# Optimization experiments

Hardware: AMD Instinct MI355X
Metric: run time of the kernel (lower is better)

Reference implementation:

```python
import jax, jax.numpy as jnp
import numpy as np

S = 4096      # total packed sequence length (8 images x 512 patches)
D = 1152      # hidden_dim
H = 16        # num_heads
HD = D // H   # head_dim = 72
MLPD = 4304   # mlp_dim
EPS = 1e-5


def setup_inputs() -> dict:
    key = jax.random.key(0)
    ks = jax.random.split(key, 16)
    f32 = jnp.float32
    w = lambda k, shp: (jax.random.normal(k, shp, f32) * 0.02)
    hidden_states = jax.random.normal(ks[0], (S, D), f32)
    cu_seqlens = (jnp.arange(9, dtype=jnp.int32) * (S // 8))  # [0,512,...,4096]
    angles = jax.random.uniform(ks[1], (S, HD // 2), f32, 0.0, 2.0 * np.pi)
    rope_cos = jnp.cos(angles)
    rope_sin = jnp.sin(angles)
    return {
        "hidden_states": hidden_states,
        "cu_seqlens": cu_seqlens,
        "rope_cos": rope_cos,
        "rope_sin": rope_sin,
        "norm0_scale": jnp.ones((D,), f32),
        "norm0_bias": jnp.zeros((D,), f32),
        "wqkv_w": w(ks[2], (D, 3 * D)),
        "wqkv_b": jnp.zeros((3 * D,), f32),
        "wo_w": w(ks[3], (D, D)),
        "wo_b": jnp.zeros((D,), f32),
        "norm1_scale": jnp.ones((D,), f32),
        "norm1_bias": jnp.zeros((D,), f32),
        "fc0_w": w(ks[4], (D, MLPD)),
        "fc0_b": jnp.zeros((MLPD,), f32),
        "fc1_w": w(ks[5], (MLPD, D)),
        "fc1_b": jnp.zeros((D,), f32),
    }


def _layernorm(x, scale, bias):
    m = jnp.mean(x, axis=-1, keepdims=True)
    v = jnp.mean(jnp.square(x - m), axis=-1, keepdims=True)
    return (x - m) * jax.lax.rsqrt(v + EPS) * scale + bias


def _rope(x, cos, sin):
    # x: (S, H, HD). Complex multiply (x0 + i x1) * (cos + i sin) in real form.
    xr = x.reshape(S, H, HD // 2, 2)
    x0, x1 = xr[..., 0], xr[..., 1]
    c = cos[:, None, :]  # (S, 1, HD/2) broadcast over heads
    s = sin[:, None, :]
    o0 = x0 * c - x1 * s
    o1 = x0 * s + x1 * c
    return jnp.stack([o0, o1], axis=-1).reshape(S, H, HD)


def _block_diag_bias(cu_seqlens):
    positions = jnp.arange(S)
    starts, ends = cu_seqlens[:-1], cu_seqlens[1:]
    in_seg = (positions[:, None] >= starts[None, :]) & (positions[:, None] < ends[None, :])
    seg = jnp.argmax(in_seg.astype(jnp.int32), axis=-1)  # (S,)
    same = seg[:, None] == seg[None, :]
    return jnp.where(same, 0.0, jnp.finfo(jnp.float32).min)  # (S, S)


def reference(hidden_states, cu_seqlens, rope_cos, rope_sin,
              norm0_scale, norm0_bias, wqkv_w, wqkv_b, wo_w, wo_b,
              norm1_scale, norm1_bias, fc0_w, fc0_b, fc1_w, fc1_b):
    # pre-norm attention block
    x = _layernorm(hidden_states, norm0_scale, norm0_bias)
    qkv = (x @ wqkv_w + wqkv_b).reshape(S, 3, H, HD)
    q, k, v = qkv[:, 0], qkv[:, 1], qkv[:, 2]
    q = _rope(q, rope_cos, rope_sin)
    k = _rope(k, rope_cos, rope_sin)
    bias = _block_diag_bias(cu_seqlens)  # (S, S)
    scale = HD ** -0.5
    scores = jnp.einsum('shd,thd->hst', q, k) * scale + bias[None, :, :]
    probs = jax.nn.softmax(scores, axis=-1)
    attn = jnp.einsum('hst,thd->shd', probs, v).reshape(S, D)
    attn = attn @ wo_w + wo_b
    h = hidden_states + attn
    # pre-norm MLP block
    y = _layernorm(h, norm1_scale, norm1_bias)
    y = jax.nn.gelu(y @ fc0_w + fc0_b) @ fc1_w + fc1_b
    return h + y
```

## Files before the change

### kernel.cpp

```cpp
#include <hip/hip_runtime.h>


#define DEV __device__ __forceinline__

typedef __attribute__((ext_vector_type(8))) short short8;
typedef __attribute__((ext_vector_type(4))) float f32x4;

typedef const void __attribute__((address_space(1))) gvoid;
typedef void __attribute__((address_space(3))) lvoid;

DEV ushort f2bf(float f) {
  union { float f; unsigned u; } x; x.f = f;
  unsigned r = (x.u + 0x7FFFu + ((x.u >> 16) & 1u)) >> 16;
  return (ushort)r;
}

DEV float bf2f(ushort u) {
  union { unsigned u; float f; } x; x.u = (unsigned)u << 16;
  return x.f;
}

DEV void gload_lds16(const void* g, void* l) {
  __builtin_amdgcn_global_load_lds((gvoid*)g, (lvoid*)l, 16, 0, 0);
}

DEV f32x4 mfma16(short8 a, short8 b, f32x4 c) {
  return __builtin_amdgcn_mfma_f32_16x16x32_bf16(a, b, c, 0, 0, 0);
}

DEV float gelu_tanh(float x) {
  float x3 = x * x * x;
  return 0.5f * x * (1.f + tanhf(0.7978845608f * (x + 0.044715f * x3)));
}

__global__ void wconv_t(const float* __restrict__ src, ushort* __restrict__ dst,
                        int K, int N, int NP, int KP) {
  __shared__ float tile[32][33];
  const int k0 = blockIdx.x * 32, n0 = blockIdx.y * 32;
  const int tx = threadIdx.x & 31, ty = threadIdx.x >> 5;
#pragma unroll
  for (int i = 0; i < 4; ++i) {
    int r = ty + i * 8;
    float v = 0.f;
    if (k0 + r < K && n0 + tx < N) v = src[(size_t)(k0 + r) * N + n0 + tx];
    tile[tx][r] = v;
  }
  __syncthreads();
#pragma unroll
  for (int i = 0; i < 4; ++i) {
    int r = ty + i * 8;
    dst[(size_t)(n0 + r) * KP + k0 + tx] = f2bf(tile[r][tx]);
  }
}

__global__ __launch_bounds__(256) void ln_bf16(const float* __restrict__ x,
                                               const float* __restrict__ sc,
                                               const float* __restrict__ bi,
                                               ushort* __restrict__ out) {
  const int row = blockIdx.x, tid = threadIdx.x;
  const float* xr = x + (size_t)row * 1152;
  const int n = (tid < 128) ? 5 : 4;
  float vals[5];
  float s = 0.f, s2 = 0.f;
#pragma unroll
  for (int i = 0; i < 5; ++i) {
    if (i < n) { float v = xr[tid + i * 256]; vals[i] = v; s += v; s2 += v * v; }
  }
#pragma unroll
  for (int off = 32; off; off >>= 1) { s += __shfl_xor(s, off); s2 += __shfl_xor(s2, off); }
  __shared__ float rs[4], rs2[4];
  if ((tid & 63) == 0) { rs[tid >> 6] = s; rs2[tid >> 6] = s2; }
  __syncthreads();
  s = rs[0] + rs[1] + rs[2] + rs[3];
  s2 = rs2[0] + rs2[1] + rs2[2] + rs2[3];
  const float mean = s * (1.f / 1152.f);
  const float var = s2 * (1.f / 1152.f) - mean * mean;
  const float rstd = rsqrtf(var + 1e-5f);
  ushort* orow = out + (size_t)row * 1152;
  for (int i = 0; i < n; ++i) {
    int c = tid + i * 256;
    orow[c] = f2bf((vals[i] - mean) * rstd * sc[c] + bi[c]);
  }
}

template <int EPI, int BN>
__global__ __launch_bounds__(256) void gemm_bt(
    const ushort* __restrict__ A, const ushort* __restrict__ Bt,
    const float* __restrict__ bias, const float* __restrict__ resid,
    float* __restrict__ outf, ushort* __restrict__ outh,
    int M, int N, int K, int n_valid) {
  __shared__ ushort lA[2][128 * 32];
  __shared__ ushort lB[2][BN * 32];
  const int tid = threadIdx.x;
  const int lane = tid & 63, wave = tid >> 6;
  const int l15 = lane & 15, lg = lane >> 4;

  const int nx = gridDim.x;
  const int nwg = nx * gridDim.y;
  int flat = blockIdx.y * nx + blockIdx.x;
  flat = (flat & 7) * (nwg >> 3) + (flat >> 3);
  const int bx = flat % nx, by = flat / nx;
  const int m0 = by * 128, n0 = bx * BN;

  constexpr int WMI = (BN == 128) ? 4 : 2;
  const int wm = (BN == 128) ? (wave >> 1) * 64 : wave * 32;
  const int wn = (BN == 128) ? (wave & 1) * 64 : 0;

  f32x4 acc[WMI][4] = {};

  const int row0 = tid >> 2, col0 = (tid & 3) << 3;
  const ushort* Ag0 = A + (size_t)(m0 + row0) * K + col0;
  const ushort* Ag1 = Ag0 + (size_t)64 * K;
  const ushort* Bg0 = Bt + (size_t)(n0 + row0) * K + col0;
  const ushort* Bg1 = Bg0 + (size_t)64 * K;

  auto stage = [&](int b, int kt) {
    gload_lds16(Ag0 + kt, &lA[b][wave * 512]);
    gload_lds16(Ag1 + kt, &lA[b][2048 + wave * 512]);
    gload_lds16(Bg0 + kt, &lB[b][wave * 512]);
    if constexpr (BN == 128) gload_lds16(Bg1 + kt, &lB[b][2048 + wave * 512]);
  };

  stage(0, 0);
  __syncthreads();
  int cur = 0;
  for (int kt = 0; kt < K; kt += 32) {
    if (kt + 32 < K) stage(cur ^ 1, kt + 32);
    short8 af[WMI], bfr[4];
#pragma unroll
    for (int i = 0; i < WMI; ++i)
      af[i] = *(const short8*)&lA[cur][(wm + i * 16 + l15) * 32 + lg * 8];
#pragma unroll
    for (int j = 0; j < 4; ++j)
      bfr[j] = *(const short8*)&lB[cur][(wn + j * 16 + l15) * 32 + lg * 8];
#pragma unroll
    for (int i = 0; i < WMI; ++i)
#pragma unroll
      for (int j = 0; j < 4; ++j)
        acc[i][j] = mfma16(af[i], bfr[j], acc[i][j]);
    __syncthreads();
    cur ^= 1;
  }

  const int cb = n0 + wn + l15;
  const int rb = m0 + wm + lg * 4;
#pragma unroll
  for (int j = 0; j < 4; ++j) {
    const int col = cb + j * 16;
    const float bv = (col < n_valid) ? bias[col] : 0.f;
#pragma unroll
    for (int i = 0; i < WMI; ++i) {
#pragma unroll
      for (int r = 0; r < 4; ++r) {
        const int row = rb + i * 16 + r;
        const size_t idx = (size_t)row * N + col;
        const float v = acc[i][j][r] + bv;
        if constexpr (EPI == 1) outf[idx] = resid[idx] + v;
        else if constexpr (EPI == 2) outh[idx] = f2bf(gelu_tanh(v));
        else outh[idx] = f2bf(v);
      }
    }
  }
}

__global__ void rope_pack(const ushort* __restrict__ qkv,
                          const float* __restrict__ cosp, const float* __restrict__ sinp,
                          ushort* __restrict__ qp, ushort* __restrict__ kp) {
  const int t = blockIdx.x * 256 + threadIdx.x;
  const int d = t % 96;
  const int hs = t / 96;
  const int h = hs & 15;
  const int s = hs >> 4;
  const size_t dst = ((size_t)h * 4096 + s) * 96 + d;
  if (d >= 72) { qp[dst] = 0; kp[dst] = 0; return; }
  const int i = d >> 1;
  const float c = cosp[s * 36 + i], sn = sinp[s * 36 + i];
  const size_t base = (size_t)s * 3456 + h * 72;
  const float q0 = bf2f(qkv[base + (d & ~1)]), q1 = bf2f(qkv[base + (d | 1)]);
  const float k0 = bf2f(qkv[base + 1152 + (d & ~1)]), k1 = bf2f(qkv[base + 1152 + (d | 1)]);
  float qo, ko;
  if ((d & 1) == 0) { qo = q0 * c - q1 * sn; ko = k0 * c - k1 * sn; }
  else              { qo = q0 * sn + q1 * c; ko = k0 * sn + k1 * c; }
  qp[dst] = f2bf(qo * 0.1178511302f);
  kp[dst] = f2bf(ko);
}

__global__ void v_pack(const ushort* __restrict__ qkv, ushort* __restrict__ vt) {
  __shared__ ushort lv[96][64];
  const int b = blockIdx.x;
  const int h = b >> 6;
  const int s0 = (b & 63) << 6;
  const int tid = threadIdx.x;
#pragma unroll
  for (int it = 0; it < 24; ++it) {
    int idx = tid + it * 256;
    int d = idx % 96, sl = idx / 96;
    lv[d][sl] = (d < 72) ? qkv[(size_t)(s0 + sl) * 3456 + 2304 + h * 72 + d] : (ushort)0;
  }
  __syncthreads();
#pragma unroll
  for (int it = 0; it < 24; ++it) {
    int idx = tid + it * 256;
    int d = idx >> 6, sl = idx & 63;
    vt[((size_t)h * 96 + d) * 4096 + s0 + sl] = lv[d][sl];
  }
}

__global__ __launch_bounds__(256) void attn_kernel(
    const ushort* __restrict__ qp, const ushort* __restrict__ kp,
    const ushort* __restrict__ vt, ushort* __restrict__ attn_out) {
  __shared__ ushort lp[4][16 * 32];
  const int tid = threadIdx.x, lane = tid & 63, wave = tid >> 6;
  const int l15 = lane & 15, lg = lane >> 4;
  const int b = blockIdx.x;
  const int h = b >> 6;
  const int rem = b & 63;
  const int seg = rem >> 3, qt = rem & 7;
  const int q0 = seg * 512 + qt * 64 + wave * 16;

  short8 aq[3];
  const ushort* qrow = qp + ((size_t)h * 4096 + q0 + l15) * 96 + lg * 8;
  aq[0] = *(const short8*)(qrow);
  aq[1] = *(const short8*)(qrow + 32);
  aq[2] = *(const short8*)(qrow + 64);

  f32x4 oacc[5] = {};
  float mrow[4] = {-1e30f, -1e30f, -1e30f, -1e30f};
  float srow[4] = {0.f, 0.f, 0.f, 0.f};

  const ushort* kbase = kp + ((size_t)h * 4096 + seg * 512) * 96;
  const ushort* vbase = vt + (size_t)h * 96 * 4096 + seg * 512;
  ushort* lpw = lp[wave];

  for (int kc = 0; kc < 16; ++kc) {
    f32x4 sc[2] = {};
#pragma unroll
    for (int n = 0; n < 2; ++n) {
      const ushort* krow = kbase + (size_t)(kc * 32 + n * 16 + l15) * 96 + lg * 8;
#pragma unroll
      for (int c = 0; c < 3; ++c) {
        short8 kb = *(const short8*)(krow + c * 32);
        sc[n] = mfma16(aq[c], kb, sc[n]);
      }
    }
    float corr[4];
#pragma unroll
    for (int j = 0; j < 4; ++j) {
      float v = fmaxf(sc[0][j], sc[1][j]);
      v = fmaxf(v, __shfl_xor(v, 1));
      v = fmaxf(v, __shfl_xor(v, 2));
      v = fmaxf(v, __shfl_xor(v, 4));
      v = fmaxf(v, __shfl_xor(v, 8));
      float mn = fmaxf(mrow[j], v);
      corr[j] = __expf(mrow[j] - mn);
      mrow[j] = mn;
    }
    float p0[4], p1[4];
#pragma unroll
    for (int j = 0; j < 4; ++j) {
      p0[j] = __expf(sc[0][j] - mrow[j]);
      p1[j] = __expf(sc[1][j] - mrow[j]);
      float ps = p0[j] + p1[j];
      ps += __shfl_xor(ps, 1);
      ps += __shfl_xor(ps, 2);
      ps += __shfl_xor(ps, 4);
      ps += __shfl_xor(ps, 8);
      srow[j] = srow[j] * corr[j] + ps;
    }
#pragma unroll
    for (int n = 0; n < 5; ++n)
#pragma unroll
      for (int j = 0; j < 4; ++j)
        oacc[n][j] *= corr[j];
#pragma unroll
    for (int j = 0; j < 4; ++j) {
      int row = lg * 4 + j;
      lpw[row * 32 + l15] = f2bf(p0[j]);
      lpw[row * 32 + 16 + l15] = f2bf(p1[j]);
    }
    __syncthreads();
    short8 pa = *(const short8*)&lpw[l15 * 32 + lg * 8];
    const ushort* vrow = vbase + kc * 32 + lg * 8;
#pragma unroll
    for (int n = 0; n < 5; ++n) {
      short8 vb = *(const short8*)(vrow + (size_t)(n * 16 + l15) * 4096);
      oacc[n] = mfma16(pa, vb, oacc[n]);
    }
    __syncthreads();
  }
#pragma unroll
  for (int j = 0; j < 4; ++j) {
    float inv = 1.f / srow[j];
    int row = q0 + lg * 4 + j;
#pragma unroll
    for (int n = 0; n < 5; ++n) {
      int col = n * 16 + l15;
      if (col < 72)
        attn_out[(size_t)row * 1152 + h * 72 + col] = f2bf(oacc[n][j] * inv);
    }
  }
}

extern "C" void kernel_launch(void* const* d_in, const int* in_sizes, int n_in,
                              void* d_out, int out_size, void* d_ws, size_t ws_size,
                              hipStream_t stream) {
  (void)in_sizes; (void)n_in; (void)out_size;
  const float* hidden = (const float*)d_in[0];
  const float* ropec = (const float*)d_in[2];
  const float* ropes = (const float*)d_in[3];
  const float* n0s = (const float*)d_in[4];
  const float* n0b = (const float*)d_in[5];
  const float* wqkv = (const float*)d_in[6];
  const float* bqkv = (const float*)d_in[7];
  const float* wo = (const float*)d_in[8];
  const float* bo = (const float*)d_in[9];
  const float* n1s = (const float*)d_in[10];
  const float* n1b = (const float*)d_in[11];
  const float* wfc0 = (const float*)d_in[12];
  const float* bfc0 = (const float*)d_in[13];
  const float* wfc1 = (const float*)d_in[14];
  const float* bfc1 = (const float*)d_in[15];
  float* out = (float*)d_out;

  char* ws = (char*)d_ws;
  ushort* x_bf   = (ushort*)(ws + 0);
  ushort* wqkv_t = (ushort*)(ws + 9437184);
  ushort* wo_t   = (ushort*)(ws + 17399808);
  ushort* fc0_t  = (ushort*)(ws + 20054016);
  ushort* fc1_t  = (ushort*)(ws + 30081024);
  ushort* qkv_bf = (ushort*)(ws + 40108032);
  ushort* mid    = (ushort*)(ws + 40108032);
  ushort* q_pad  = (ushort*)(ws + 96731136);
  ushort* k_pad  = (ushort*)(ws + 109314048);
  ushort* vt     = (ushort*)(ws + 121896960);
  ushort* attn   = (ushort*)(ws + 134479872);
  float*  hbuf   = (float*)(ws + 143917056);
  ushort* yln    = (ushort*)(ws + 162791424);
  if (ws_size < 172228608) return;

  wconv_t<<<dim3(36, 108), 256, 0, stream>>>(wqkv, wqkv_t, 1152, 3456, 3456, 1152);
  wconv_t<<<dim3(36, 36), 256, 0, stream>>>(wo, wo_t, 1152, 1152, 1152, 1152);
  wconv_t<<<dim3(36, 136), 256, 0, stream>>>(wfc0, fc0_t, 1152, 4304, 4352, 1152);
  wconv_t<<<dim3(136, 36), 256, 0, stream>>>(wfc1, fc1_t, 4304, 1152, 1152, 4352);

  ln_bf16<<<4096, 256, 0, stream>>>(hidden, n0s, n0b, x_bf);

  gemm_bt<3, 128><<<dim3(27, 32), 256, 0, stream>>>(x_bf, wqkv_t, bqkv, nullptr, nullptr, qkv_bf,
                                                    4096, 3456, 1152, 3456);
  rope_pack<<<24576, 256, 0, stream>>>(qkv_bf, ropec, ropes, q_pad, k_pad);
  v_pack<<<1024, 256, 0, stream>>>(qkv_bf, vt);

  attn_kernel<<<1024, 256, 0, stream>>>(q_pad, k_pad, vt, attn);

  gemm_bt<1, 64><<<dim3(18, 32), 256, 0, stream>>>(attn, wo_t, bo, hidden, hbuf, nullptr,
                                                   4096, 1152, 1152, 1152);
  ln_bf16<<<4096, 256, 0, stream>>>(hbuf, n1s, n1b, yln);

  gemm_bt<2, 128><<<dim3(34, 32), 256, 0, stream>>>(yln, fc0_t, bfc0, nullptr, nullptr, mid,
                                                    4096, 4352, 1152, 4304);
  gemm_bt<1, 64><<<dim3(18, 32), 256, 0, stream>>>(mid, fc1_t, bfc1, hbuf, out, nullptr,
                                                   4096, 1152, 4352, 1152);
}
```

Baseline: 393.9 us.

## Enlarge GEMM tiles to 256x128 and deepen K step to 64

Reworks the bf16 GEMM so each workgroup covers a 256x128 tile with 512 threads for the QKV and fc0 projections, and a 128x128 tile for the output and fc1 projections. The K loop now stages 64-wide slices per buffer with two MFMA sub-steps, halving the number of barriers and raising arithmetic intensity per LDS fill. Load addressing is generalized into per-thread row offset arrays. In exchange, LDS use and register pressure go up, and the grids get smaller (e.g. 288 blocks for the N=1152 GEMMs), which may underfill the 256 CUs.

```diff
diff --git a/kernel.cpp b/kernel.cpp
--- a/kernel.cpp
+++ b/kernel.cpp
@@ -83,14 +83,17 @@
   }
 }
 
-template <int EPI, int BN>
-__global__ __launch_bounds__(256) void gemm_bt(
+template <int EPI, int BM>
+__global__ __launch_bounds__(BM == 256 ? 512 : 256, 2) void gemm_bt(
     const ushort* __restrict__ A, const ushort* __restrict__ Bt,
     const float* __restrict__ bias, const float* __restrict__ resid,
     float* __restrict__ outf, ushort* __restrict__ outh,
-    int M, int N, int K, int n_valid) {
-  __shared__ ushort lA[2][128 * 32];
-  __shared__ ushort lB[2][BN * 32];
+    int N, int K, int n_valid) {
+  constexpr int T = (BM == 256) ? 512 : 256;
+  constexpr int LOADS_A = BM * 8 / T;
+  constexpr int LOADS_B = 128 * 8 / T;
+  __shared__ ushort lA[2][BM * 64];
+  __shared__ ushort lB[2][128 * 64];
   const int tid = threadIdx.x;
   const int lane = tid & 63, wave = tid >> 6;
   const int l15 = lane & 15, lg = lane >> 4;
@@ -100,44 +103,54 @@
   int flat = blockIdx.y * nx + blockIdx.x;
   flat = (flat & 7) * (nwg >> 3) + (flat >> 3);
   const int bx = flat % nx, by = flat / nx;
-  const int m0 = by * 128, n0 = bx * BN;
-
-  constexpr int WMI = (BN == 128) ? 4 : 2;
-  const int wm = (BN == 128) ? (wave >> 1) * 64 : wave * 32;
-  const int wn = (BN == 128) ? (wave & 1) * 64 : 0;
-
-  f32x4 acc[WMI][4] = {};
-
-  const int row0 = tid >> 2, col0 = (tid & 3) << 3;
-  const ushort* Ag0 = A + (size_t)(m0 + row0) * K + col0;
-  const ushort* Ag1 = Ag0 + (size_t)64 * K;
-  const ushort* Bg0 = Bt + (size_t)(n0 + row0) * K + col0;
-  const ushort* Bg1 = Bg0 + (size_t)64 * K;
+  const int m0 = by * BM, n0 = bx * 128;
+
+  const int wm = (wave >> 1) * 64;
+  const int wn = (wave & 1) * 64;
+
+  f32x4 acc[4][4] = {};
+
+  size_t arow[LOADS_A], brow[LOADS_B];
+#pragma unroll
+  for (int i = 0; i < LOADS_A; ++i) {
+    int c = i * T + tid;
+    arow[i] = (size_t)(m0 + (c >> 3)) * K + (c & 7) * 8;
+  }
+#pragma unroll
+  for (int i = 0; i < LOADS_B; ++i) {
+    int c = i * T + tid;
+    brow[i] = (size_t)(n0 + (c >> 3)) * K + (c & 7) * 8;
+  }
 
   auto stage = [&](int b, int kt) {
-    gload_lds16(Ag0 + kt, &lA[b][wave * 512]);
-    gload_lds16(Ag1 + kt, &lA[b][2048 + wave * 512]);
-    gload_lds16(Bg0 + kt, &lB[b][wave * 512]);
-    if constexpr (BN == 128) gload_lds16(Bg1 + kt, &lB[b][2048 + wave * 512]);
+#pragma unroll
+    for (int i = 0; i < LOADS_A; ++i)
+      gload_lds16(A + arow[i] + kt, &lA[b][(i * T + wave * 64) * 8]);
+#pragma unroll
+    for (int i = 0; i < LOADS_B; ++i)
+      gload_lds16(Bt + brow[i] + kt, &lB[b][(i * T + wave * 64) * 8]);
   };
 
   stage(0, 0);
   __syncthreads();
   int cur = 0;
-  for (int kt = 0; kt < K; kt += 32) {
-    if (kt + 32 < K) stage(cur ^ 1, kt + 32);
-    short8 af[WMI], bfr[4];
-#pragma unroll
-    for (int i = 0; i < WMI; ++i)
-      af[i] = *(const short8*)&lA[cur][(wm + i * 16 + l15) * 32 + lg * 8];
-#pragma unroll
-    for (int j = 0; j < 4; ++j)
-      bfr[j] = *(const short8*)&lB[cur][(wn + j * 16 + l15) * 32 + lg * 8];
-#pragma unroll
-    for (int i = 0; i < WMI; ++i)
+  for (int kt = 0; kt < K; kt += 64) {
+    if (kt + 64 < K) stage(cur ^ 1, kt + 64);
+#pragma unroll
+    for (int ks = 0; ks < 2; ++ks) {
+      short8 af[4], bfr[4];
+#pragma unroll
+      for (int i = 0; i < 4; ++i)
+        af[i] = *(const short8*)&lA[cur][(wm + i * 16 + l15) * 64 + ks * 32 + lg * 8];
 #pragma unroll
       for (int j = 0; j < 4; ++j)
-        acc[i][j] = mfma16(af[i], bfr[j], acc[i][j]);
+        bfr[j] = *(const short8*)&lB[cur][(wn + j * 16 + l15) * 64 + ks * 32 + lg * 8];
+#pragma unroll
+      for (int i = 0; i < 4; ++i)
+#pragma unroll
+        for (int j = 0; j < 4; ++j)
+          acc[i][j] = mfma16(af[i], bfr[j], acc[i][j]);
+    }
     __syncthreads();
     cur ^= 1;
   }
@@ -149,7 +162,7 @@
     const int col = cb + j * 16;
     const float bv = (col < n_valid) ? bias[col] : 0.f;
 #pragma unroll
-    for (int i = 0; i < WMI; ++i) {
+    for (int i = 0; i < 4; ++i) {
 #pragma unroll
       for (int r = 0; r < 4; ++r) {
         const int row = rb + i * 16 + r;
@@ -345,19 +358,19 @@
 
   ln_bf16<<<4096, 256, 0, stream>>>(hidden, n0s, n0b, x_bf);
 
-  gemm_bt<3, 128><<<dim3(27, 32), 256, 0, stream>>>(x_bf, wqkv_t, bqkv, nullptr, nullptr, qkv_bf,
-                                                    4096, 3456, 1152, 3456);
+  gemm_bt<3, 256><<<dim3(27, 16), 512, 0, stream>>>(x_bf, wqkv_t, bqkv, nullptr, nullptr, qkv_bf,
+                                                    3456, 1152, 3456);
   rope_pack<<<24576, 256, 0, stream>>>(qkv_bf, ropec, ropes, q_pad, k_pad);
   v_pack<<<1024, 256, 0, stream>>>(qkv_bf, vt);
 
   attn_kernel<<<1024, 256, 0, stream>>>(q_pad, k_pad, vt, attn);
 
-  gemm_bt<1, 64><<<dim3(18, 32), 256, 0, stream>>>(attn, wo_t, bo, hidden, hbuf, nullptr,
-                                                   4096, 1152, 1152, 1152);
+  gemm_bt<1, 128><<<dim3(9, 32), 256, 0, stream>>>(attn, wo_t, bo, hidden, hbuf, nullptr,
+                                                   1152, 1152, 1152);
   ln_bf16<<<4096, 256, 0, stream>>>(hbuf, n1s, n1b, yln);
 
-  gemm_bt<2, 128><<<dim3(34, 32), 256, 0, stream>>>(yln, fc0_t, bfc0, nullptr, nullptr, mid,
-                                                    4096, 4352, 1152, 4304);
-  gemm_bt<1, 64><<<dim3(18, 32), 256, 0, stream>>>(mid, fc1_t, bfc1, hbuf, out, nullptr,
-                                                   4096, 1152, 4352, 1152);
-}
+  gemm_bt<2, 256><<<dim3(34, 16), 512, 0, stream>>>(yln, fc0_t, bfc0, nullptr, nullptr, mid,
+                                                    4352, 1152, 4304);
+  gemm_bt<1, 128><<<dim3(9, 32), 256, 0, stream>>>(mid, fc1_t, bfc1, hbuf, out, nullptr,
+                                                   1152, 4352, 1152);
+}
```

Measured after the change: 446.6 us. 1.13x slower.

## Replace GEMMs with 256x128 triple-buffered swizzled kernel and split-K for fc1

Applied to the files above, without the earlier changes.

Replaces the 128xBN double-buffered GEMM with a 512-thread, 256x128-tile kernel using a K-step of 64, three LDS stages, XOR-swizzled LDS layout, register double-buffered fragments and raised wave priority around the MFMA block. The fc1 GEMM is split along K into two partial outputs that a separate vectorized kernel sums with bias and residual. The goal is more reuse per tile, fewer LDS bank conflicts and better overlap of loads with MFMA. In exchange it uses much more LDS per block, which limits occupancy, and split-K adds an extra pass over the output in memory.

```diff
diff --git a/kernel.cpp b/kernel.cpp
--- a/kernel.cpp
+++ b/kernel.cpp
@@ -83,83 +83,137 @@
   }
 }
 
-template <int EPI, int BN>
-__global__ __launch_bounds__(256) void gemm_bt(
+template <int EPI>
+__global__ __launch_bounds__(512, 2) void gemm_p(
     const ushort* __restrict__ A, const ushort* __restrict__ Bt,
     const float* __restrict__ bias, const float* __restrict__ resid,
     float* __restrict__ outf, ushort* __restrict__ outh,
-    int M, int N, int K, int n_valid) {
-  __shared__ ushort lA[2][128 * 32];
-  __shared__ ushort lB[2][BN * 32];
+    int N, int Kstride, int NT, int n_valid) {
+  __shared__ ushort L[3][24576];
   const int tid = threadIdx.x;
   const int lane = tid & 63, wave = tid >> 6;
   const int l15 = lane & 15, lg = lane >> 4;
 
-  const int nx = gridDim.x;
-  const int nwg = nx * gridDim.y;
-  int flat = blockIdx.y * nx + blockIdx.x;
+  const int nx = gridDim.x, ny = gridDim.y;
+  const int nwg = nx * ny * gridDim.z;
+  int flat = (blockIdx.z * ny + blockIdx.y) * nx + blockIdx.x;
   flat = (flat & 7) * (nwg >> 3) + (flat >> 3);
-  const int bx = flat % nx, by = flat / nx;
-  const int m0 = by * 128, n0 = bx * BN;
-
-  constexpr int WMI = (BN == 128) ? 4 : 2;
-  const int wm = (BN == 128) ? (wave >> 1) * 64 : wave * 32;
-  const int wn = (BN == 128) ? (wave & 1) * 64 : 0;
-
-  f32x4 acc[WMI][4] = {};
-
-  const int row0 = tid >> 2, col0 = (tid & 3) << 3;
-  const ushort* Ag0 = A + (size_t)(m0 + row0) * K + col0;
-  const ushort* Ag1 = Ag0 + (size_t)64 * K;
-  const ushort* Bg0 = Bt + (size_t)(n0 + row0) * K + col0;
-  const ushort* Bg1 = Bg0 + (size_t)64 * K;
-
-  auto stage = [&](int b, int kt) {
-    gload_lds16(Ag0 + kt, &lA[b][wave * 512]);
-    gload_lds16(Ag1 + kt, &lA[b][2048 + wave * 512]);
-    gload_lds16(Bg0 + kt, &lB[b][wave * 512]);
-    if constexpr (BN == 128) gload_lds16(Bg1 + kt, &lB[b][2048 + wave * 512]);
+  const int bx = flat % nx;
+  const int rem = flat / nx;
+  const int by = rem % ny;
+  const int bz = rem / ny;
+  const int m0 = by * 256, n0 = bx * 128;
+  const int k0 = bz * NT * 64;
+
+  const int swz = ((tid & 7) ^ ((tid >> 3) & 7)) * 8;
+  const int rstg = tid >> 3;
+  const ushort* Ag = A + (size_t)(m0 + rstg) * Kstride + k0 + swz;
+  const ushort* Bg = Bt + (size_t)(n0 + rstg) * Kstride + k0 + swz;
+
+  auto stage = [&](int b, int t) {
+    ushort* d = &L[b][0];
+#pragma unroll
+    for (int i = 0; i < 4; ++i)
+      gload_lds16(Ag + ((size_t)i * 64) * Kstride + t * 64,
+                  d + (i * 512 + wave * 64) * 8);
+#pragma unroll
+    for (int i = 0; i < 2; ++i)
+      gload_lds16(Bg + ((size_t)i * 64) * Kstride + t * 64,
+                  d + 16384 + (i * 512 + wave * 64) * 8);
   };
 
-  stage(0, 0);
-  __syncthreads();
-  int cur = 0;
-  for (int kt = 0; kt < K; kt += 32) {
-    if (kt + 32 < K) stage(cur ^ 1, kt + 32);
-    short8 af[WMI], bfr[4];
-#pragma unroll
-    for (int i = 0; i < WMI; ++i)
-      af[i] = *(const short8*)&lA[cur][(wm + i * 16 + l15) * 32 + lg * 8];
-#pragma unroll
-    for (int j = 0; j < 4; ++j)
-      bfr[j] = *(const short8*)&lB[cur][(wn + j * 16 + l15) * 32 + lg * 8];
-#pragma unroll
-    for (int i = 0; i < WMI; ++i)
-#pragma unroll
-      for (int j = 0; j < 4; ++j)
-        acc[i][j] = mfma16(af[i], bfr[j], acc[i][j]);
-    __syncthreads();
-    cur ^= 1;
-  }
-
+  const int wm = (wave >> 1) * 64, wn = (wave & 1) * 64;
+  const int cph0 = (lg ^ (l15 & 7)) * 8;
+  const int cph1 = ((4 + lg) ^ (l15 & 7)) * 8;
+
+  auto rdfrag = [&](int b, short8 (&fa)[4][2], short8 (&fb)[4][2]) {
+    const ushort* la = &L[b][0];
+    const ushort* lb = &L[b][16384];
+#pragma unroll
+    for (int mf = 0; mf < 4; ++mf) {
+      fa[mf][0] = *(const short8*)&la[(wm + mf * 16 + l15) * 64 + cph0];
+      fa[mf][1] = *(const short8*)&la[(wm + mf * 16 + l15) * 64 + cph1];
+    }
+#pragma unroll
+    for (int nf = 0; nf < 4; ++nf) {
+      fb[nf][0] = *(const short8*)&lb[(wn + nf * 16 + l15) * 64 + cph0];
+      fb[nf][1] = *(const short8*)&lb[(wn + nf * 16 + l15) * 64 + cph1];
+    }
+  };
+
+  f32x4 acc[4][4] = {};
+  short8 fa[2][4][2], fb[2][4][2];
+
+  stage(0, 0); stage(1, 1); stage(2, 2);
+  asm volatile("s_waitcnt vmcnt(6)" ::: "memory");
+  __builtin_amdgcn_s_barrier();
+  rdfrag(0, fa[0], fb[0]);
+
+  int b0 = 0, b1 = 1;
+
+#define GBODY(TT, CUR, NXT)                                                   \
+  {                                                                           \
+    const int _t = (TT);                                                      \
+    if (_t + 1 < NT) rdfrag(b1, fa[NXT], fb[NXT]);                            \
+    if (_t + 3 < NT) stage(b0, _t + 3);                                       \
+    __builtin_amdgcn_s_setprio(1);                                            \
+    _Pragma("unroll") for (int mf = 0; mf < 4; ++mf)                          \
+      _Pragma("unroll") for (int nf = 0; nf < 4; ++nf) {                      \
+        acc[mf][nf] = mfma16(fa[CUR][mf][0], fb[CUR][nf][0], acc[mf][nf]);    \
+        acc[mf][nf] = mfma16(fa[CUR][mf][1], fb[CUR][nf][1], acc[mf][nf]);    \
+      }                                                                       \
+    __builtin_amdgcn_s_setprio(0);                                            \
+    asm volatile("s_waitcnt lgkmcnt(0)" ::: "memory");                        \
+    __builtin_amdgcn_sched_barrier(0);                                        \
+    if (_t + 3 < NT) { asm volatile("s_waitcnt vmcnt(6)" ::: "memory"); }     \
+    else if (_t + 2 < NT) { asm volatile("s_waitcnt vmcnt(0)" ::: "memory"); }\
+    if (_t + 1 < NT) __builtin_amdgcn_s_barrier();                            \
+    const int _b2 = 3 - b0 - b1; b0 = b1; b1 = _b2;                           \
+  }
+
+  for (int t = 0; t < NT; t += 2) {
+    GBODY(t, 0, 1);
+    GBODY(t + 1, 1, 0);
+  }
+#undef GBODY
+
+  float* outp = outf;
+  if constexpr (EPI == 0) outp = outf + (size_t)bz * ((size_t)4096 * N);
   const int cb = n0 + wn + l15;
   const int rb = m0 + wm + lg * 4;
 #pragma unroll
   for (int j = 0; j < 4; ++j) {
     const int col = cb + j * 16;
-    const float bv = (col < n_valid) ? bias[col] : 0.f;
-#pragma unroll
-    for (int i = 0; i < WMI; ++i) {
+    const float bv = (EPI != 0 && col < n_valid) ? bias[col] : 0.f;
+#pragma unroll
+    for (int i = 0; i < 4; ++i) {
 #pragma unroll
       for (int r = 0; r < 4; ++r) {
         const int row = rb + i * 16 + r;
         const size_t idx = (size_t)row * N + col;
         const float v = acc[i][j][r] + bv;
-        if constexpr (EPI == 1) outf[idx] = resid[idx] + v;
+        if constexpr (EPI == 0) outp[idx] = v;
+        else if constexpr (EPI == 1) outf[idx] = resid[idx] + v;
         else if constexpr (EPI == 2) outh[idx] = f2bf(gelu_tanh(v));
         else outh[idx] = f2bf(v);
       }
     }
+  }
+}
+
+__global__ __launch_bounds__(256) void ksum_reduce(
+    const float* __restrict__ hb, const float* __restrict__ bias,
+    const float* __restrict__ p0, const float* __restrict__ p1,
+    float* __restrict__ out) {
+  const f32x4* hb4 = (const f32x4*)hb;
+  const f32x4* b4 = (const f32x4*)bias;
+  const f32x4* p04 = (const f32x4*)p0;
+  const f32x4* p14 = (const f32x4*)p1;
+  f32x4* o4 = (f32x4*)out;
+  const int total = 4096 * 288;
+  for (int i = blockIdx.x * 256 + threadIdx.x; i < total; i += gridDim.x * 256) {
+    f32x4 r = hb4[i] + b4[i % 288] + p04[i] + p14[i];
+    o4[i] = r;
   }
 }
 
@@ -333,6 +387,7 @@
   ushort* q_pad  = (ushort*)(ws + 96731136);
   ushort* k_pad  = (ushort*)(ws + 109314048);
   ushort* vt     = (ushort*)(ws + 121896960);
+  float*  pbuf   = (float*)(ws + 96731136);
   ushort* attn   = (ushort*)(ws + 134479872);
   float*  hbuf   = (float*)(ws + 143917056);
   ushort* yln    = (ushort*)(ws + 162791424);
@@ -345,19 +400,20 @@
 
   ln_bf16<<<4096, 256, 0, stream>>>(hidden, n0s, n0b, x_bf);
 
-  gemm_bt<3, 128><<<dim3(27, 32), 256, 0, stream>>>(x_bf, wqkv_t, bqkv, nullptr, nullptr, qkv_bf,
-                                                    4096, 3456, 1152, 3456);
+  gemm_p<3><<<dim3(27, 16), 512, 0, stream>>>(x_bf, wqkv_t, bqkv, nullptr, nullptr, qkv_bf,
+                                              3456, 1152, 18, 3456);
   rope_pack<<<24576, 256, 0, stream>>>(qkv_bf, ropec, ropes, q_pad, k_pad);
   v_pack<<<1024, 256, 0, stream>>>(qkv_bf, vt);
 
   attn_kernel<<<1024, 256, 0, stream>>>(q_pad, k_pad, vt, attn);
 
-  gemm_bt<1, 64><<<dim3(18, 32), 256, 0, stream>>>(attn, wo_t, bo, hidden, hbuf, nullptr,
-                                                   4096, 1152, 1152, 1152);
+  gemm_p<1><<<dim3(9, 16), 512, 0, stream>>>(attn, wo_t, bo, hidden, hbuf, nullptr,
+                                             1152, 1152, 18, 1152);
   ln_bf16<<<4096, 256, 0, stream>>>(hbuf, n1s, n1b, yln);
 
-  gemm_bt<2, 128><<<dim3(34, 32), 256, 0, stream>>>(yln, fc0_t, bfc0, nullptr, nullptr, mid,
-                                                    4096, 4352, 1152, 4304);
-  gemm_bt<1, 64><<<dim3(18, 32), 256, 0, stream>>>(mid, fc1_t, bfc1, hbuf, out, nullptr,
-                                                   4096, 1152, 4352, 1152);
-}
+  gemm_p<2><<<dim3(34, 16), 512, 0, stream>>>(yln, fc0_t, bfc0, nullptr, nullptr, mid,
+                                              4352, 1152, 18, 4304);
+  gemm_p<0><<<dim3(9, 16, 2), 512, 0, stream>>>(mid, fc1_t, nullptr, nullptr, pbuf, nullptr,
+                                                1152, 4352, 34, 1152);
+  ksum_reduce<<<2048, 256, 0, stream>>>(hbuf, bfc1, pbuf, pbuf + (size_t)4096 * 1152, out);
+}
```

Result: faster. 378.3 us (-4.0%).
